# Performance work log

Hardware: AMD Instinct MI355X
Metric: run time of the kernel (lower is better)

Reference implementation:

```python
import jax, jax.numpy as jnp
import numpy as np

D_MODEL = 1024
NUM_HEADS = 8
D_K = D_MODEL // NUM_HEADS
NEG_INF = -1e9
EPS = 1e-6


def setup_inputs() -> dict:
    key = jax.random.key(0)
    ks = jax.random.split(key, 10)
    B, S = 4, 2048
    scale = 1.0 / np.sqrt(D_MODEL)
    return {
        "queries": jax.random.normal(ks[0], (B, S, D_MODEL), jnp.float32),
        "keys": jax.random.normal(ks[1], (B, S, D_MODEL), jnp.float32),
        "values": jax.random.normal(ks[2], (B, S, D_MODEL), jnp.float32),
        "Wq": jax.random.normal(ks[3], (D_MODEL, D_MODEL), jnp.float32) * scale,
        "bq": jnp.zeros((D_MODEL,), jnp.float32),
        "Wk": jax.random.normal(ks[4], (D_MODEL, D_MODEL), jnp.float32) * scale,
        "bk": jnp.zeros((D_MODEL,), jnp.float32),
        "Wv": jax.random.normal(ks[5], (D_MODEL, D_MODEL), jnp.float32) * scale,
        "bv": jnp.zeros((D_MODEL,), jnp.float32),
        "gamma": jnp.ones((D_MODEL,), jnp.float32),
        "beta": jnp.zeros((D_MODEL,), jnp.float32),
    }


def _split_heads(x, B, S):
    # [B,S,D] -> [B,H,S,d_k]
    return x.reshape(B, S, NUM_HEADS, D_K).transpose(0, 2, 1, 3)


def reference(queries, keys, values, Wq, bq, Wk, bk, Wv, bv, gamma, beta):
    B, S, _ = queries.shape
    Q = _split_heads(queries @ Wq + bq, B, S)
    K = _split_heads(keys @ Wk + bk, B, keys.shape[1])
    V = _split_heads(values @ Wv + bv, B, values.shape[1])
    scores = jnp.einsum("bhqd,bhkd->bhqk", Q, K) / jnp.sqrt(jnp.float32(D_K))
    # causal mask (lower triangular kept)
    Sk = scores.shape[-1]
    mask = jnp.tril(jnp.ones((scores.shape[-2], Sk), dtype=bool))
    scores = jnp.where(mask, scores, jnp.float32(NEG_INF))
    attn = jax.nn.softmax(scores, axis=-1)
    # dropout disabled (training=False)
    out = jnp.einsum("bhqk,bhkd->bhqd", attn, V)
    out = out.transpose(0, 2, 1, 3).reshape(B, S, D_MODEL)
    resid = out + queries
    mu = jnp.mean(resid, axis=-1, keepdims=True)
    var = jnp.var(resid, axis=-1, keepdims=True)
    normed = (resid - mu) / jnp.sqrt(var + EPS)
    return normed * gamma + beta
```

## Files before the change

### kernel.cpp

```cpp
#include <hip/hip_runtime.h>
#include <hip/hip_bf16.h>
#include <stdint.h>

#define D_MODEL 1024
#define S_LEN   2048
#define BATCH   4
#define NH      8
#define DK      128

typedef __attribute__((ext_vector_type(8))) __bf16 bf16x8;
typedef __attribute__((ext_vector_type(4))) float  f32x4;

__device__ __forceinline__ f32x4 mfma16(bf16x8 a, bf16x8 b, f32x4 c) {
  return __builtin_amdgcn_mfma_f32_16x16x32_bf16(a, b, c, 0, 0, 0);
}

__device__ __forceinline__ void gld_lds16(const void* g, void* l) {
  __builtin_amdgcn_global_load_lds(
      (const __attribute__((address_space(1))) void*)g,
      (__attribute__((address_space(3))) void*)l, 16, 0, 0);
}

#define ATTN_SCALE 0.08838834764831845f

__global__ __launch_bounds__(256) void cvt_kernel(
    const float* __restrict__ x0, const float* __restrict__ x1,
    const float* __restrict__ x2, __hip_bfloat16* __restrict__ out) {
  const size_t N = (size_t)BATCH * S_LEN * D_MODEL;
  const int w = blockIdx.y;
  const float* src = (w == 0) ? x0 : (w == 1) ? x1 : x2;
  __hip_bfloat16* dst = out + (size_t)w * N;
  const size_t i = ((size_t)blockIdx.x * 256 + threadIdx.x) * 4;
  const float4 v = *(const float4*)(src + i);
  *(__hip_bfloat162*)(dst + i)     = __float22bfloat162_rn(make_float2(v.x, v.y));
  *(__hip_bfloat162*)(dst + i + 2) = __float22bfloat162_rn(make_float2(v.z, v.w));
}

__global__ void wtrans_kernel(const float* __restrict__ Wq,
                              const float* __restrict__ Wk,
                              const float* __restrict__ Wv,
                              __hip_bfloat16* __restrict__ Wt) {
  __shared__ __hip_bfloat16 tile[32][33];
  const int w = blockIdx.z;
  const float* src = (w == 0) ? Wq : (w == 1) ? Wk : Wv;
  const float sc = (w == 0) ? ATTN_SCALE : 1.0f;
  __hip_bfloat16* dst = Wt + (size_t)w * D_MODEL * D_MODEL;
  const int tx = threadIdx.x, ty = threadIdx.y;
  int x = blockIdx.x * 32 + tx;
  int y = blockIdx.y * 32 + ty;
  for (int i = 0; i < 32; i += 8)
    tile[ty + i][tx] = __float2bfloat16(src[(size_t)(y + i) * D_MODEL + x] * sc);
  __syncthreads();
  x = blockIdx.y * 32 + tx;
  y = blockIdx.x * 32 + ty;
  for (int i = 0; i < 32; i += 8)
    dst[(size_t)(y + i) * D_MODEL + x] = tile[tx][ty + i];
}

__global__ __launch_bounds__(256) void qkv_gemm_kernel(
    const __hip_bfloat16* __restrict__ Xbf,
    const float* __restrict__ bq, const float* __restrict__ bk,
    const float* __restrict__ bv,
    const __hip_bfloat16* __restrict__ Wt,
    __hip_bfloat16* __restrict__ Qo, __hip_bfloat16* __restrict__ Ko,
    __hip_bfloat16* __restrict__ Vo) {
  const int flat = blockIdx.x;
  const int xcd  = flat & 7;
  const int idx  = flat >> 3;
  const int n_t  = idx & 7;
  const int mg   = idx >> 3;
  const int pair = xcd * 24 + mg;
  const int which = pair >> 6;
  const int m_t   = pair & 63;

  const size_t N = (size_t)BATCH * S_LEN * D_MODEL;
  const __hip_bfloat16* X = Xbf + (size_t)which * N;
  const __hip_bfloat16* W = Wt + (size_t)which * D_MODEL * D_MODEL;
  const float* bias = (which == 0) ? bq : (which == 1) ? bk : bv;
  const float bscale = (which == 0) ? ATTN_SCALE : 1.0f;

  __shared__ __align__(16) __hip_bfloat16 Asm[128 * 32];
  __shared__ __align__(16) __hip_bfloat16 Bsm[128 * 32];

  const int tid  = threadIdx.x;
  const int lane = tid & 63;
  const int wv   = tid >> 6;
  const int lo16 = lane & 15;
  const int hi4  = lane >> 4;
  const int m0 = m_t * 128;
  const int n0 = n_t * 128;
  const int wm = (wv >> 1) * 64;
  const int wn = (wv & 1) * 64;

  f32x4 acc[4][4];
  const f32x4 z4 = {0.f, 0.f, 0.f, 0.f};
  for (int i = 0; i < 4; ++i)
    for (int j = 0; j < 4; ++j) acc[i][j] = z4;

  for (int k0 = 0; k0 < D_MODEL; k0 += 32) {
    __syncthreads();
    for (int it = 0; it < 2; ++it) {
      const int cbase = it * 256 + wv * 64;
      const int c = cbase + lane;
      gld_lds16(X + (size_t)(m0 + (c >> 2)) * D_MODEL + k0 + (c & 3) * 8,
                &Asm[cbase * 8]);
      gld_lds16(W + (size_t)(n0 + (c >> 2)) * D_MODEL + k0 + (c & 3) * 8,
                &Bsm[cbase * 8]);
    }
    __syncthreads();

    bf16x8 af[4], bfr[4];
    for (int i = 0; i < 4; ++i)
      af[i] = *(const bf16x8*)&Asm[(wm + 16 * i + lo16) * 32 + hi4 * 8];
    for (int j = 0; j < 4; ++j)
      bfr[j] = *(const bf16x8*)&Bsm[(wn + 16 * j + lo16) * 32 + hi4 * 8];
    for (int i = 0; i < 4; ++i)
      for (int j = 0; j < 4; ++j)
        acc[i][j] = mfma16(af[i], bfr[j], acc[i][j]);
  }

  const int b = m0 >> 11;
  for (int j = 0; j < 4; ++j) {
    const int n = n0 + wn + j * 16 + lo16;
    const float bval = bias[n] * bscale;
    const int h = n >> 7;
    const int d = n & 127;
    for (int i = 0; i < 4; ++i) {
      for (int r = 0; r < 4; ++r) {
        const int m = m0 + wm + 16 * i + hi4 * 4 + r;
        const int s = m & (S_LEN - 1);
        const __hip_bfloat16 ob = __float2bfloat16(acc[i][j][r] + bval);
        const size_t bh = (size_t)(b * NH + h);
        if (which == 0) {
          Qo[(bh * S_LEN + s) * DK + d] = ob;
        } else if (which == 1) {
          Ko[(bh * 64 + (s >> 5)) * 4096 + (d >> 3) * 256 + (s & 31) * 8 +
             (d & 7)] = ob;
        } else {
          Vo[(bh * 64 + (s >> 5)) * 4096 + ((s & 31) >> 3) * 1024 + d * 8 +
             (s & 7)] = ob;
        }
      }
    }
  }
}

__device__ const uint32_t ATTN_TBL[24] = {
  79, 95, 32,
  78, 94, 33,
  77, 93, 34,
  76, 92, 35,
  75, 91, 36,
  39, 72, 88,
  38, 73, 89,
  37, 74, 90
};

__global__ __launch_bounds__(256) void attn_kernel(
    const __hip_bfloat16* __restrict__ Qw, const __hip_bfloat16* __restrict__ Kw,
    const __hip_bfloat16* __restrict__ Vtw, __hip_bfloat16* __restrict__ Og,
    float* __restrict__ partO, float* __restrict__ lsumP) {
  const int bid = blockIdx.x;
  const int q8  = bid & 255;
  const int rr  = bid >> 8;
  const int bh  = q8 & 31;
  const int jrow = q8 >> 5;
  const int h   = bh & 7;
  const int b   = bh >> 3;
  const uint32_t wi = ATTN_TBL[jrow * 3 + rr];
  const int  t     = wi & 15;
  const int  chnk  = (wi >> 4) & 1;
  const bool split = (wi >> 5) == 2;
  const int  half  = 2 * t + 2;
  const int  st0   = (split && chnk == 1) ? half : 0;
  const int  stN   = (split && chnk == 0) ? half : (4 * t + 4);

  const int tid  = threadIdx.x;
  const int lane = tid & 63;
  const int wv   = tid >> 6;
  const int lo16 = lane & 15;
  const int hi4  = lane >> 4;

  const int qrow0 = t * 128 + wv * 32;
  const int ns_w  = 4 * t + wv + 1;

  const size_t bhp = (size_t)(b * NH + h);
  const __hip_bfloat16* Qp = Qw + bhp * S_LEN * DK;
  const __hip_bfloat16* Kp = Kw + bhp * S_LEN * DK;
  const __hip_bfloat16* Vp = Vtw + bhp * S_LEN * DK;

  __shared__ __align__(16) __hip_bfloat16 Ksm[2][32 * 128];
  __shared__ __align__(16) __hip_bfloat16 Vsm[2][128 * 32];
  __shared__ __align__(16) __hip_bfloat16 Psm[4][32 * 40];

  bf16x8 qf[2][4];
  for (int m = 0; m < 2; ++m)
    for (int kk = 0; kk < 4; ++kk)
      qf[m][kk] = *(const bf16x8*)&Qp[(size_t)(qrow0 + m * 16 + lo16) * DK +
                                      kk * 32 + hi4 * 8];

  f32x4 oacc[2][8];
  const f32x4 z4 = {0.f, 0.f, 0.f, 0.f};
  for (int m = 0; m < 2; ++m)
    for (int j = 0; j < 8; ++j) oacc[m][j] = z4;
  float lsum[2][4];
  for (int m = 0; m < 2; ++m)
    for (int i = 0; i < 4; ++i) lsum[m][i] = 0.f;

  const __hip_bfloat16* kbase[2];
  const __hip_bfloat16* vbase[2];
#pragma unroll
  for (int it = 0; it < 2; ++it) {
    const int c = it * 256 + tid;
    kbase[it] = Kp + (size_t)c * 8;
    vbase[it] = Vp + (size_t)c * 8;
  }
  auto stage = [&](int st, int buf) {
#pragma unroll
    for (int it = 0; it < 2; ++it) {
      const int cb = (it * 256 + wv * 64) * 8;
      gld_lds16(kbase[it] + ((size_t)st << 12), &Ksm[buf][cb]);
      gld_lds16(vbase[it] + ((size_t)st << 12), &Vsm[buf][cb]);
    }
  };

  stage(st0, 0);

  int bsel = 0;
  for (int st = st0; st < stN; ++st) {
    asm volatile("s_waitcnt vmcnt(0)" ::: "memory");
    __builtin_amdgcn_s_barrier();
    asm volatile("" ::: "memory");
    if (st + 1 < stN) stage(st + 1, bsel ^ 1);

    if (st < ns_w) {
      const __hip_bfloat16* Kb = Ksm[bsel];
      const __hip_bfloat16* Vb = Vsm[bsel];

      bf16x8 kf[2][4];
      for (int kn = 0; kn < 2; ++kn)
        for (int kk = 0; kk < 4; ++kk)
          kf[kn][kk] = *(const bf16x8*)&Kb[((kk * 4 + hi4) * 32 + kn * 16 + lo16) * 8];
      f32x4 sc[2][2];
      for (int m = 0; m < 2; ++m)
        for (int kn = 0; kn < 2; ++kn) {
          f32x4 s4 = z4;
          for (int kk = 0; kk < 4; ++kk)
            s4 = mfma16(qf[m][kk], kf[kn][kk], s4);
          sc[m][kn] = s4;
        }

      const int kv0 = st << 5;
      const bool do_mask = (st == ns_w - 1);
      for (int m = 0; m < 2; ++m) {
        for (int i = 0; i < 4; ++i) {
          const int qg = qrow0 + m * 16 + hi4 * 4 + i;
          float s0 = sc[m][0][i];
          float s1 = sc[m][1][i];
          if (do_mask) {
            if (kv0 + lo16 > qg)      s0 = -1.0e30f;
            if (kv0 + 16 + lo16 > qg) s1 = -1.0e30f;
          }
          const float p0 = __expf(s0 - 8.f);
          const float p1 = __expf(s1 - 8.f);
          lsum[m][i] += p0 + p1;
          const int prw = m * 16 + hi4 * 4 + i;
          Psm[wv][prw * 40 + lo16]      = __float2bfloat16(p0);
          Psm[wv][prw * 40 + 16 + lo16] = __float2bfloat16(p1);
        }
      }
      asm volatile("s_waitcnt lgkmcnt(0)" ::: "memory");

      bf16x8 pf[2];
      for (int m = 0; m < 2; ++m)
        pf[m] = *(const bf16x8*)&Psm[wv][(m * 16 + lo16) * 40 + hi4 * 8];
      for (int j = 0; j < 8; ++j) {
        const bf16x8 vf = *(const bf16x8*)&Vb[(hi4 * 128 + j * 16 + lo16) * 8];
        oacc[0][j] = mfma16(pf[0], vf, oacc[0][j]);
        oacc[1][j] = mfma16(pf[1], vf, oacc[1][j]);
      }
    }
    bsel ^= 1;
  }

  for (int m = 0; m < 2; ++m) {
    for (int i = 0; i < 4; ++i) {
      float l = lsum[m][i];
      l += __shfl_xor(l, 1);
      l += __shfl_xor(l, 2);
      l += __shfl_xor(l, 4);
      l += __shfl_xor(l, 8);
      const int row = wv * 32 + m * 16 + hi4 * 4 + i;
      if (!split) {
        const float inv = 1.0f / l;
        const int qg = t * 128 + row;
        __hip_bfloat16* orow = Og + ((size_t)b * S_LEN + qg) * D_MODEL + h * DK;
        for (int j = 0; j < 8; ++j)
          orow[j * 16 + lo16] = __float2bfloat16(oacc[m][j][i] * inv);
      } else {
        const int pidx = bh * 8 + (t - 8);
        float* prow = partO +
            (((size_t)chnk * 256 + pidx) * 128 + row) * 128;
        for (int j = 0; j < 8; ++j)
          prow[j * 16 + lo16] = oacc[m][j][i];
        if (lo16 == 0)
          lsumP[(chnk * 256 + pidx) * 128 + row] = l;
      }
    }
  }
}

__global__ __launch_bounds__(256) void ln_kernel(
    const __hip_bfloat16* __restrict__ Og, const float* __restrict__ partO,
    const float* __restrict__ lsumP, const float* __restrict__ resid_in,
    const float* __restrict__ gamma, const float* __restrict__ beta,
    float* __restrict__ out) {
  const int row  = blockIdx.x;
  const int b    = row >> 11;
  const int srow = row & (S_LEN - 1);
  const int tile = srow >> 7;
  const int tid  = threadIdx.x;
  const int base = tid * 4;
  const float4 q4 = *(const float4*)(resid_in + (size_t)row * D_MODEL + base);
  float v[4];
  if (tile < 8) {
    const __hip_bfloat16* orow = Og + (size_t)row * D_MODEL;
    const ushort4 o4 = *(const ushort4*)(orow + base);
    v[0] = __bfloat162float(*(const __hip_bfloat16*)&o4.x) + q4.x;
    v[1] = __bfloat162float(*(const __hip_bfloat16*)&o4.y) + q4.y;
    v[2] = __bfloat162float(*(const __hip_bfloat16*)&o4.z) + q4.z;
    v[3] = __bfloat162float(*(const __hip_bfloat16*)&o4.w) + q4.w;
  } else {
    const int h    = base >> 7;
    const int rin  = srow & 127;
    const int pidx = (b * 8 + h) * 8 + (tile - 8);
    const size_t off = ((size_t)pidx * 128 + rin) * 128 + (base & 127);
    const float4 p0 = *(const float4*)(partO + off);
    const float4 p1 = *(const float4*)(partO + (size_t)256 * 128 * 128 + off);
    const float l = lsumP[pidx * 128 + rin] +
                    lsumP[256 * 128 + pidx * 128 + rin];
    const float inv = 1.0f / l;
    v[0] = (p0.x + p1.x) * inv + q4.x;
    v[1] = (p0.y + p1.y) * inv + q4.y;
    v[2] = (p0.z + p1.z) * inv + q4.z;
    v[3] = (p0.w + p1.w) * inv + q4.w;
  }
  float s = v[0] + v[1] + v[2] + v[3];
  float ss = v[0] * v[0] + v[1] * v[1] + v[2] * v[2] + v[3] * v[3];
  for (int m = 1; m < 64; m <<= 1) { s += __shfl_xor(s, m); ss += __shfl_xor(ss, m); }
  __shared__ float red[8];
  const int wv = tid >> 6, lane = tid & 63;
  if (lane == 0) { red[wv] = s; red[4 + wv] = ss; }
  __syncthreads();
  s  = red[0] + red[1] + red[2] + red[3];
  ss = red[4] + red[5] + red[6] + red[7];
  const float mu  = s * (1.0f / D_MODEL);
  const float var = ss * (1.0f / D_MODEL) - mu * mu;
  const float rstd = rsqrtf(var + 1e-6f);
  const float4 g4 = *(const float4*)(gamma + base);
  const float4 b4 = *(const float4*)(beta + base);
  float4 o;
  o.x = (v[0] - mu) * rstd * g4.x + b4.x;
  o.y = (v[1] - mu) * rstd * g4.y + b4.y;
  o.z = (v[2] - mu) * rstd * g4.z + b4.z;
  o.w = (v[3] - mu) * rstd * g4.w + b4.w;
  *(float4*)(out + (size_t)row * D_MODEL + base) = o;
}

extern "C" void kernel_launch(void* const* d_in, const int* in_sizes, int n_in,
                              void* d_out, int out_size, void* d_ws, size_t ws_size,
                              hipStream_t stream) {
  const float* queries = (const float*)d_in[0];
  const float* keys    = (const float*)d_in[1];
  const float* values  = (const float*)d_in[2];
  const float* Wq = (const float*)d_in[3];
  const float* bq = (const float*)d_in[4];
  const float* Wk = (const float*)d_in[5];
  const float* bk = (const float*)d_in[6];
  const float* Wv = (const float*)d_in[7];
  const float* bv = (const float*)d_in[8];
  const float* gamma = (const float*)d_in[9];
  const float* beta  = (const float*)d_in[10];

  char* ws = (char*)d_ws;
  const size_t N = (size_t)BATCH * S_LEN * D_MODEL;
  const size_t WT_BYTES  = (size_t)3 * D_MODEL * D_MODEL * 2;
  const size_t XBF_BYTES = (size_t)3 * N * 2;
  const size_t QKV_BYTES = (size_t)BATCH * NH * S_LEN * DK * 2;
  const size_t OG_BYTES  = (size_t)BATCH * S_LEN * D_MODEL * 2;
  __hip_bfloat16* Wt  = (__hip_bfloat16*)ws;
  __hip_bfloat16* Xbf = (__hip_bfloat16*)(ws + WT_BYTES);
  __hip_bfloat16* Ogs = (__hip_bfloat16*)(ws + WT_BYTES);
  float* partO = (float*)(ws + WT_BYTES + OG_BYTES);
  float* lsumP = (float*)ws;
  __hip_bfloat16* Qws = (__hip_bfloat16*)(ws + WT_BYTES + XBF_BYTES);
  __hip_bfloat16* Kws = (__hip_bfloat16*)(ws + WT_BYTES + XBF_BYTES + QKV_BYTES);
  __hip_bfloat16* Vws = (__hip_bfloat16*)(ws + WT_BYTES + XBF_BYTES + 2 * QKV_BYTES);

  cvt_kernel<<<dim3((unsigned)(N / 1024), 3), 256, 0, stream>>>(queries, keys, values, Xbf);
  wtrans_kernel<<<dim3(32, 32, 3), dim3(32, 8), 0, stream>>>(Wq, Wk, Wv, Wt);
  qkv_gemm_kernel<<<dim3(1536), 256, 0, stream>>>(
      Xbf, bq, bk, bv, Wt, Qws, Kws, Vws);
  attn_kernel<<<dim3(768), 256, 0, stream>>>(Qws, Kws, Vws, Ogs, partO, lsumP);
  ln_kernel<<<dim3(BATCH * S_LEN), 256, 0, stream>>>(Ogs, partO, lsumP, queries,
                                                     gamma, beta, (float*)d_out);
}
```

Baseline: 347.5 us.

## Swizzle projection GEMM LDS, stage epilogue through LDS, pack P stores

The QKV projection kernel now loads a K-depth of 64 per iteration into an XOR-swizzled LDS layout, which halves the number of barrier rounds and avoids bank conflicts on fragment reads. Its epilogue now writes accumulators into a padded LDS tile and then issues coalesced 16-byte global stores for the Q, K and V layouts, replacing scattered 2-byte stores. In attention, the two P values per lane are written as one packed bf16 pair. To keep P·V correct, the V tile's sequence order inside each 32-key block is permuted to match. This costs extra LDS traffic and barriers in the epilogue, and it couples the V layout to the P layout.

Result: faster. 325.0 us (-6.5%).

```diff
diff --git a/kernel.cpp b/kernel.cpp
--- a/kernel.cpp
+++ b/kernel.cpp
@@ -79,8 +79,10 @@
   const float* bias = (which == 0) ? bq : (which == 1) ? bk : bv;
   const float bscale = (which == 0) ? ATTN_SCALE : 1.0f;
 
-  __shared__ __align__(16) __hip_bfloat16 Asm[128 * 32];
-  __shared__ __align__(16) __hip_bfloat16 Bsm[128 * 32];
+  __shared__ __align__(16) char smem[128 * 136 * 2];
+  __hip_bfloat16* Asm = (__hip_bfloat16*)smem;
+  __hip_bfloat16* Bsm = Asm + 128 * 64;
+  __hip_bfloat16* Cb  = (__hip_bfloat16*)smem;
 
   const int tid  = threadIdx.x;
   const int lane = tid & 63;
@@ -97,50 +99,83 @@
   for (int i = 0; i < 4; ++i)
     for (int j = 0; j < 4; ++j) acc[i][j] = z4;
 
-  for (int k0 = 0; k0 < D_MODEL; k0 += 32) {
+  for (int k0 = 0; k0 < D_MODEL; k0 += 64) {
     __syncthreads();
-    for (int it = 0; it < 2; ++it) {
+    for (int it = 0; it < 4; ++it) {
       const int cbase = it * 256 + wv * 64;
       const int c = cbase + lane;
-      gld_lds16(X + (size_t)(m0 + (c >> 2)) * D_MODEL + k0 + (c & 3) * 8,
-                &Asm[cbase * 8]);
-      gld_lds16(W + (size_t)(n0 + (c >> 2)) * D_MODEL + k0 + (c & 3) * 8,
-                &Bsm[cbase * 8]);
+      const int row = c >> 3;
+      const int kc = ((c & 7) ^ (row & 7)) * 8;
+      gld_lds16(X + (size_t)(m0 + row) * D_MODEL + k0 + kc, &Asm[cbase * 8]);
+      gld_lds16(W + (size_t)(n0 + row) * D_MODEL + k0 + kc, &Bsm[cbase * 8]);
     }
     __syncthreads();
 
-    bf16x8 af[4], bfr[4];
-    for (int i = 0; i < 4; ++i)
-      af[i] = *(const bf16x8*)&Asm[(wm + 16 * i + lo16) * 32 + hi4 * 8];
-    for (int j = 0; j < 4; ++j)
-      bfr[j] = *(const bf16x8*)&Bsm[(wn + 16 * j + lo16) * 32 + hi4 * 8];
-    for (int i = 0; i < 4; ++i)
-      for (int j = 0; j < 4; ++j)
-        acc[i][j] = mfma16(af[i], bfr[j], acc[i][j]);
-  }
-
-  const int b = m0 >> 11;
+    for (int kk = 0; kk < 2; ++kk) {
+      bf16x8 af[4], bfr[4];
+      const int sl = (kk * 4 + hi4);
+      for (int i = 0; i < 4; ++i) {
+        const int lm = wm + 16 * i + lo16;
+        af[i] = *(const bf16x8*)&Asm[lm * 64 + ((sl ^ (lm & 7)) * 8)];
+      }
+      for (int j = 0; j < 4; ++j) {
+        const int ln = wn + 16 * j + lo16;
+        bfr[j] = *(const bf16x8*)&Bsm[ln * 64 + ((sl ^ (ln & 7)) * 8)];
+      }
+      for (int i = 0; i < 4; ++i)
+        for (int j = 0; j < 4; ++j)
+          acc[i][j] = mfma16(af[i], bfr[j], acc[i][j]);
+    }
+  }
+
+  const int b  = m0 >> 11;
+  const int s0 = m0 & (S_LEN - 1);
+  const int h  = n0 >> 7;
+  const size_t bh = (size_t)(b * NH + h);
+
+  __syncthreads();
   for (int j = 0; j < 4; ++j) {
-    const int n = n0 + wn + j * 16 + lo16;
-    const float bval = bias[n] * bscale;
-    const int h = n >> 7;
-    const int d = n & 127;
+    const int nl = wn + 16 * j + lo16;
+    const float bval = bias[n0 + nl] * bscale;
     for (int i = 0; i < 4; ++i) {
       for (int r = 0; r < 4; ++r) {
-        const int m = m0 + wm + 16 * i + hi4 * 4 + r;
-        const int s = m & (S_LEN - 1);
+        const int lm = wm + 16 * i + hi4 * 4 + r;
         const __hip_bfloat16 ob = __float2bfloat16(acc[i][j][r] + bval);
-        const size_t bh = (size_t)(b * NH + h);
-        if (which == 0) {
-          Qo[(bh * S_LEN + s) * DK + d] = ob;
-        } else if (which == 1) {
-          Ko[(bh * 64 + (s >> 5)) * 4096 + (d >> 3) * 256 + (s & 31) * 8 +
-             (d & 7)] = ob;
+        if (which == 2) {
+          const int col = (lm & 96) + 2 * (lm & 15) + ((lm >> 4) & 1);
+          Cb[nl * 136 + col] = ob;
         } else {
-          Vo[(bh * 64 + (s >> 5)) * 4096 + ((s & 31) >> 3) * 1024 + d * 8 +
-             (s & 7)] = ob;
+          Cb[lm * 136 + nl] = ob;
         }
       }
+    }
+  }
+  __syncthreads();
+
+  if (which == 0) {
+    __hip_bfloat16* gq = Qo + (bh * S_LEN + s0) * DK;
+    for (int r8 = 0; r8 < 8; ++r8) {
+      const int C = r8 * 256 + tid;
+      const bf16x8 v = *(const bf16x8*)&Cb[(C >> 4) * 136 + (C & 15) * 8];
+      *(bf16x8*)&gq[(size_t)C * 8] = v;
+    }
+  } else if (which == 1) {
+    __hip_bfloat16* gk = Ko + (bh * 64 + (s0 >> 5)) * 4096;
+    for (int r8 = 0; r8 < 8; ++r8) {
+      const int C = r8 * 256 + tid;
+      const int su = C >> 9, Cw = C & 511;
+      const bf16x8 v =
+          *(const bf16x8*)&Cb[(su * 32 + (Cw & 31)) * 136 + (Cw >> 5) * 8];
+      *(bf16x8*)&gk[(size_t)su * 4096 + (Cw >> 5) * 256 + (Cw & 31) * 8] = v;
+    }
+  } else {
+    __hip_bfloat16* gv = Vo + (bh * 64 + (s0 >> 5)) * 4096;
+    for (int r8 = 0; r8 < 8; ++r8) {
+      const int C = r8 * 256 + tid;
+      const int su = C >> 9, Cw = C & 511;
+      const bf16x8 v =
+          *(const bf16x8*)&Cb[(C & 127) * 136 + su * 32 + (Cw >> 7) * 8];
+      *(bf16x8*)&gv[(size_t)su * 4096 + (size_t)Cw * 8] = v;
     }
   }
 }
@@ -265,8 +300,8 @@
           const float p1 = __expf(s1 - 8.f);
           lsum[m][i] += p0 + p1;
           const int prw = m * 16 + hi4 * 4 + i;
-          Psm[wv][prw * 40 + lo16]      = __float2bfloat16(p0);
-          Psm[wv][prw * 40 + 16 + lo16] = __float2bfloat16(p1);
+          *(__hip_bfloat162*)&Psm[wv][prw * 40 + 2 * lo16] =
+              __float22bfloat162_rn(make_float2(p0, p1));
         }
       }
       asm volatile("s_waitcnt lgkmcnt(0)" ::: "memory");
```
